# Performance work log

Measured on AMD Instinct MI355X. Metric: run time of the kernel, lower is better.

## Reference

```python
import jax, jax.numpy as jnp
import numpy as np

NEG = -10000.0


def _build_label_vocab():
    vocab = {'O': 0}
    i = 1
    for t in ['PER', 'ORG', 'LOC', 'MISC']:
        for p in ['B', 'I', 'E', 'S']:
            vocab[f'{p}-{t}'] = i
            i += 1
    return vocab


def _init_transition(key):
    """Random transition with BIOES constraints, matching CRF.initialize()."""
    vocab = _build_label_vocab()
    L = len(vocab) + 2          # 19 (17 labels + start + end)
    start, end = L - 2, L - 1
    T = np.array(jax.random.normal(key, (L, L)), dtype=np.float32)
    T[:, end] = NEG
    T[start, :] = NEG
    for lf, i_f in vocab.items():
        pf, tf = ('O', 'O') if lf == 'O' else lf.split('-')
        for lt, i_t in vocab.items():
            pt, tt = ('O', 'O') if lt == 'O' else lt.split('-')
            allowed = (pf in ('O', 'E', 'S') and pt in ('O', 'B', 'S')) or \
                      (pf in ('B', 'I') and pt in ('I', 'E') and tf == tt)
            if not allowed:
                T[i_t, i_f] = NEG
    return jnp.asarray(T)


def setup_inputs() -> dict:
    key = jax.random.key(0)
    k1, k2, k3, k4 = jax.random.split(key, 4)
    B, S, NL = 4096, 256, 17
    logits = jax.random.normal(k1, (B, S, NL), dtype=jnp.float32)
    labels = jax.random.randint(k2, (B, S), 0, NL)
    lens = jax.random.randint(k3, (B,), 1, S + 1)   # lengths in [1, S]
    transition = _init_transition(k4)                # [19, 19]
    return {"logits": logits, "labels": labels, "lens": lens,
            "transition": transition}


def reference(logits, labels, lens, transition):
    """CRF log-likelihood: gold_score(pad_logits(logits)) - norm_score."""
    B, S, NL = logits.shape
    L = transition.shape[0]       # label_size = NL + 2
    start, end = L - 2, L - 1

    # pad_logits: append start/end columns with -10000
    pads = jnp.full((B, S, 2), NEG, dtype=logits.dtype)
    logits_p = jnp.concatenate([logits, pads], axis=2)   # [B, S, L]

    tmask = (jnp.arange(S)[None, :] < lens[:, None])     # [B, S] valid tokens

    # ---- gold score ----
    # unary: gather emission score of the gold label at each position
    unary = jnp.take_along_axis(logits_p, labels[:, :, None], axis=2)[:, :, 0]
    unary = (unary * tmask.astype(logits.dtype)).sum(axis=1)

    # binary: transition scores along the gold path (with start/end padding)
    labels_ext = jnp.concatenate(
        [jnp.full((B, 1), start, labels.dtype), labels,
         jnp.full((B, 1), end, labels.dtype)], axis=1)   # [B, S+2]
    emask = jnp.arange(S + 2)[None, :] < (lens + 1)[:, None]
    labels_ext = jnp.where(emask, labels_ext, end)
    trn_scr = transition[labels_ext[:, 1:], labels_ext[:, :-1]]  # [B, S+1]
    bmask = (jnp.arange(S + 1)[None, :] < (lens + 1)[:, None]).astype(logits.dtype)
    binary = (trn_scr * bmask).sum(axis=1)

    gold = unary + binary

    # ---- partition (norm) score: forward algorithm over time ----
    alpha0 = jnp.full((B, L), NEG, dtype=logits.dtype).at[:, start].set(0.0)

    def step(alpha, xs):
        logit, m = xs  # logit: [B, L], m: [B] bool (position < len)
        # alpha_nxt[b,i] = logit[b,i] + LSE_j(alpha[b,j] + T[i,j])
        nxt = logit + jax.nn.logsumexp(alpha[:, None, :] + transition[None], axis=2)
        alpha = jnp.where(m[:, None], nxt, alpha)
        return alpha, None

    alpha, _ = jax.lax.scan(step, alpha0,
                            (jnp.swapaxes(logits_p, 0, 1), tmask.T))
    alpha = alpha + transition[end][None, :]
    norm = jax.nn.logsumexp(alpha, axis=1)

    return gold - norm   # [B] per-sequence log-likelihood
```

## Files before the change

### kernel.cpp

```cpp
#include <hip/hip_runtime.h>

constexpr int S  = 256;
constexpr int NL = 17;
constexpr int L  = 19;

__global__ __launch_bounds__(64)
void crf_fwd(const float* __restrict__ logits,
             const int*   __restrict__ labels,
             const int*   __restrict__ lens,
             const float* __restrict__ transition,
             float* __restrict__ out)
{
    __shared__ float Tsh[L * L];
    __shared__ __align__(16) float pbuf[2][2][20];

    const int tid  = threadIdx.x;
    const int half = tid >> 5;
    const int lane = tid & 31;
    const int b    = (blockIdx.x << 1) + half;

    for (int k = tid; k < L * L; k += 64) Tsh[k] = transition[k];
    __syncthreads();

    const int  i   = lane;
    const bool act = (i < L);
    const int  ic  = act ? i : 0;

    float Erow[L];
    #pragma unroll
    for (int j = 0; j < L; ++j) Erow[j] = __expf(Tsh[ic * L + j]);

    const int len = lens[b];
    int mlv = max(len, __shfl_xor(len, 32));
    const int maxlen  = __builtin_amdgcn_readfirstlane(mlv);
    const int maxlen8 = (maxlen + 7) & ~7;

    const float* lgp  = logits + (size_t)b * S * NL;
    const int*   labp = labels + (size_t)b * S;

    float p = (i == L - 2) ? 1.0f : 0.0f;
    float m    = 0.0f;
    float utot = 0.0f;
    float btot = 0.0f;
    int prevlab = L - 2;

    float lgbuf[8];
    int   labbuf[8];
    #pragma unroll
    for (int u = 0; u < 8; ++u) {
        lgbuf[u]  = (i < NL) ? lgp[u * NL + i] : 0.0f;
        labbuf[u] = labp[u];
    }

    for (int tb = 0; tb < maxlen8; tb += 8) {
        #pragma unroll
        for (int u = 0; u < 8; ++u) {
            const int   t   = tb + u;
            const float lg  = lgbuf[u];
            const int   lab = labbuf[u];
            const int   tn  = (t + 8 < S) ? (t + 8) : (S - 1);
            lgbuf[u]  = (i < NL) ? lgp[tn * NL + i] : 0.0f;
            labbuf[u] = labp[tn];

            const bool upd = (t < len);

            utot += (upd && i == lab) ? lg : 0.0f;
            const float gtr = Tsh[lab * L + prevlab];
            btot += upd ? gtr : 0.0f;
            prevlab = upd ? lab : prevlab;

            const float el = (i < NL) ? __expf(lg) : 0.0f;

            float* pb = &pbuf[half][u & 1][0];
            if (act) pb[i] = p;
            asm volatile("s_waitcnt lgkmcnt(0)" ::: "memory");
            const float4* q = (const float4*)pb;
            const float4 q0 = q[0], q1 = q[1], q2 = q[2], q3 = q[3], q4 = q[4];

            float a0 = q0.x * Erow[0];
            float a1 = q0.y * Erow[1];
            float a2 = q0.z * Erow[2];
            float a3 = q0.w * Erow[3];
            a0 = fmaf(q1.x, Erow[4],  a0);
            a1 = fmaf(q1.y, Erow[5],  a1);
            a2 = fmaf(q1.z, Erow[6],  a2);
            a3 = fmaf(q1.w, Erow[7],  a3);
            a0 = fmaf(q2.x, Erow[8],  a0);
            a1 = fmaf(q2.y, Erow[9],  a1);
            a2 = fmaf(q2.z, Erow[10], a2);
            a3 = fmaf(q2.w, Erow[11], a3);
            a0 = fmaf(q3.x, Erow[12], a0);
            a1 = fmaf(q3.y, Erow[13], a1);
            a2 = fmaf(q3.z, Erow[14], a2);
            a3 = fmaf(q3.w, Erow[15], a3);
            a0 = fmaf(q4.x, Erow[16], a0);
            a1 = fmaf(q4.y, Erow[17], a1);
            a2 = fmaf(q4.z, Erow[18], a2);

            float v  = (a0 + a1) + (a2 + a3);
            float pn = v * el;

            if ((t & 3) == 3) {
                float m0 = fmaxf(fmaxf(q0.x, q0.y), fmaxf(q0.z, q0.w));
                float m1 = fmaxf(fmaxf(q1.x, q1.y), fmaxf(q1.z, q1.w));
                float m2 = fmaxf(fmaxf(q2.x, q2.y), fmaxf(q2.z, q2.w));
                float m3 = fmaxf(fmaxf(q3.x, q3.y), fmaxf(q3.z, q3.w));
                float m4 = fmaxf(fmaxf(q4.x, q4.y), q4.z);
                float mx = fmaxf(fmaxf(m0, m1), fmaxf(fmaxf(m2, m3), m4));
                pn *= __frcp_rn(mx);
                if (upd) m += __logf(mx);
            }
            p = upd ? pn : p;
        }
    }

    const float Eend = __expf(Tsh[(L - 1) * L + ic]);
    float term = act ? p * Eend : 0.0f;
    #pragma unroll
    for (int off = 16; off >= 1; off >>= 1)
        term += __shfl_xor(term, off, 32);
    const float norm = m + __logf(term);

    #pragma unroll
    for (int off = 16; off >= 1; off >>= 1)
        utot += __shfl_xor(utot, off, 32);
    const int lastlab = labp[len - 1];
    const float gold = utot + btot + Tsh[(L - 1) * L + lastlab];

    if (lane == 0) out[b] = gold - norm;
}

extern "C" void kernel_launch(void* const* d_in, const int* in_sizes, int n_in,
                              void* d_out, int out_size, void* d_ws, size_t ws_size,
                              hipStream_t stream)
{
    (void)n_in; (void)out_size; (void)d_ws; (void)ws_size;
    const float* logits     = (const float*)d_in[0];
    const int*   labels     = (const int*)d_in[1];
    const int*   lens       = (const int*)d_in[2];
    const float* transition = (const float*)d_in[3];
    float*       out        = (float*)d_out;
    const int B = in_sizes[2];
    crf_fwd<<<dim3(B / 2), dim3(64), 0, stream>>>(logits, labels, lens, transition, out);
}
```

Measured before the change: 149.0 us.

## Split each sequence into forward and backward halves computed by two half-waves

Each sequence is now handled by one 64-lane wave instead of one 32-lane half. The first half-wave runs the forward recursion over the first len/2 tokens, and the second half-wave runs a backward recursion from the end token using the transposed transition. The two results are combined with a dot product across halves, and the gold score is also split across the halves. This roughly halves the serial dependency chain per sequence and removes the per-pair max-length imbalance. In exchange it doubles the lane count per sequence, so total thread work and the number of waves launched roughly double.

```diff
diff --git a/kernel.cpp b/kernel.cpp
--- a/kernel.cpp
+++ b/kernel.cpp
@@ -3,8 +3,9 @@
 constexpr int S  = 256;
 constexpr int NL = 17;
 constexpr int L  = 19;
+constexpr int WPB = 2;
 
-__global__ __launch_bounds__(64)
+__global__ __launch_bounds__(64 * WPB)
 void crf_fwd(const float* __restrict__ logits,
              const int*   __restrict__ labels,
              const int*   __restrict__ lens,
@@ -12,93 +13,117 @@
              float* __restrict__ out)
 {
     __shared__ float Tsh[L * L];
-    __shared__ __align__(16) float pbuf[2][2][20];
+    __shared__ __align__(16) float pbuf[WPB][2][2][20];
 
     const int tid  = threadIdx.x;
-    const int half = tid >> 5;
-    const int lane = tid & 31;
-    const int b    = (blockIdx.x << 1) + half;
+    const int wave = tid >> 6;
+    const int wtid = tid & 63;
+    const int half = wtid >> 5;
+    const int lane = wtid & 31;
+    const int b    = blockIdx.x * WPB + wave;
 
-    for (int k = tid; k < L * L; k += 64) Tsh[k] = transition[k];
+    for (int k = tid; k < L * L; k += 64 * WPB) Tsh[k] = transition[k];
     __syncthreads();
 
     const int  i   = lane;
     const bool act = (i < L);
     const int  ic  = act ? i : 0;
 
-    float Erow[L];
+    float coef[L];
     #pragma unroll
-    for (int j = 0; j < L; ++j) Erow[j] = __expf(Tsh[ic * L + j]);
+    for (int j = 0; j < L; ++j)
+        coef[j] = __expf(half ? Tsh[j * L + ic] : Tsh[ic * L + j]);
 
     const int len = lens[b];
-    int mlv = max(len, __shfl_xor(len, 32));
-    const int maxlen  = __builtin_amdgcn_readfirstlane(mlv);
-    const int maxlen8 = (maxlen + 7) & ~7;
+    const int mid = len >> 1;
+    const int nf  = mid;
+    const int nb  = len - mid;
+    const int nup = half ? nb : nf;
+    const int nsteps8 = (nb + 7) & ~7;
 
     const float* lgp  = logits + (size_t)b * S * NL;
     const int*   labp = labels + (size_t)b * S;
 
-    float p = (i == L - 2) ? 1.0f : 0.0f;
+    float p = half ? (act ? __expf(Tsh[(L - 1) * L + ic]) : 0.0f)
+                   : ((i == L - 2) ? 1.0f : 0.0f);
     float m    = 0.0f;
     float utot = 0.0f;
     float btot = 0.0f;
-    int prevlab = L - 2;
+    int   prevF = L - 2;
+
+    if (half) btot = Tsh[(L - 1) * L + labp[len - 1]];
 
     float lgbuf[8];
     int   labbuf[8];
     #pragma unroll
     for (int u = 0; u < 8; ++u) {
-        lgbuf[u]  = (i < NL) ? lgp[u * NL + i] : 0.0f;
-        labbuf[u] = labp[u];
+        int tb0 = len - 1 - u; tb0 = (tb0 > 0) ? tb0 : 0;
+        const int tok = half ? tb0 : u;
+        lgbuf[u]  = (i < NL) ? lgp[tok * NL + i] : 0.0f;
+        labbuf[u] = labp[tok];
     }
 
-    for (int tb = 0; tb < maxlen8; tb += 8) {
+    for (int tb = 0; tb < nsteps8; tb += 8) {
         #pragma unroll
         for (int u = 0; u < 8; ++u) {
             const int   t   = tb + u;
             const float lg  = lgbuf[u];
             const int   lab = labbuf[u];
-            const int   tn  = (t + 8 < S) ? (t + 8) : (S - 1);
-            lgbuf[u]  = (i < NL) ? lgp[tn * NL + i] : 0.0f;
-            labbuf[u] = labp[tn];
+            const int   labnxt = labbuf[(u + 1) & 7];
+            {
+                int tpf = t + 8;       tpf = (tpf < S) ? tpf : (S - 1);
+                int tpb = len - 9 - t; tpb = (tpb > 0) ? tpb : 0;
+                const int tok = half ? tpb : tpf;
+                lgbuf[u]  = (i < NL) ? lgp[tok * NL + i] : 0.0f;
+                labbuf[u] = labp[tok];
+            }
+            const bool upd = (t < nup);
 
-            const bool upd = (t < len);
-
+            int prv;
+            if (half) {
+                const int utok = len - 1 - t;
+                prv = (utok >= 1) ? labnxt : (L - 2);
+            } else {
+                prv = prevF;
+            }
             utot += (upd && i == lab) ? lg : 0.0f;
-            const float gtr = Tsh[lab * L + prevlab];
+            const float gtr = Tsh[lab * L + prv];
             btot += upd ? gtr : 0.0f;
-            prevlab = upd ? lab : prevlab;
+            prevF = upd ? lab : prevF;
 
             const float el = (i < NL) ? __expf(lg) : 0.0f;
+            const float pe = p * el;
+            const float wv = half ? pe : p;
 
-            float* pb = &pbuf[half][u & 1][0];
-            if (act) pb[i] = p;
+            float* pb = &pbuf[wave][half][u & 1][0];
+            if (act) pb[i] = wv;
             asm volatile("s_waitcnt lgkmcnt(0)" ::: "memory");
             const float4* q = (const float4*)pb;
             const float4 q0 = q[0], q1 = q[1], q2 = q[2], q3 = q[3], q4 = q[4];
 
-            float a0 = q0.x * Erow[0];
-            float a1 = q0.y * Erow[1];
-            float a2 = q0.z * Erow[2];
-            float a3 = q0.w * Erow[3];
-            a0 = fmaf(q1.x, Erow[4],  a0);
-            a1 = fmaf(q1.y, Erow[5],  a1);
-            a2 = fmaf(q1.z, Erow[6],  a2);
-            a3 = fmaf(q1.w, Erow[7],  a3);
-            a0 = fmaf(q2.x, Erow[8],  a0);
-            a1 = fmaf(q2.y, Erow[9],  a1);
-            a2 = fmaf(q2.z, Erow[10], a2);
-            a3 = fmaf(q2.w, Erow[11], a3);
-            a0 = fmaf(q3.x, Erow[12], a0);
-            a1 = fmaf(q3.y, Erow[13], a1);
-            a2 = fmaf(q3.z, Erow[14], a2);
-            a3 = fmaf(q3.w, Erow[15], a3);
-            a0 = fmaf(q4.x, Erow[16], a0);
-            a1 = fmaf(q4.y, Erow[17], a1);
-            a2 = fmaf(q4.z, Erow[18], a2);
+            float a0 = q0.x * coef[0];
+            float a1 = q0.y * coef[1];
+            float a2 = q0.z * coef[2];
+            float a3 = q0.w * coef[3];
+            a0 = fmaf(q1.x, coef[4],  a0);
+            a1 = fmaf(q1.y, coef[5],  a1);
+            a2 = fmaf(q1.z, coef[6],  a2);
+            a3 = fmaf(q1.w, coef[7],  a3);
+            a0 = fmaf(q2.x, coef[8],  a0);
+            a1 = fmaf(q2.y, coef[9],  a1);
+            a2 = fmaf(q2.z, coef[10], a2);
+            a3 = fmaf(q2.w, coef[11], a3);
+            a0 = fmaf(q3.x, coef[12], a0);
+            a1 = fmaf(q3.y, coef[13], a1);
+            a2 = fmaf(q3.z, coef[14], a2);
+            a3 = fmaf(q3.w, coef[15], a3);
+            a0 = fmaf(q4.x, coef[16], a0);
+            a1 = fmaf(q4.y, coef[17], a1);
+            a2 = fmaf(q4.z, coef[18], a2);
 
-            float v  = (a0 + a1) + (a2 + a3);
-            float pn = v * el;
+            const float v   = (a0 + a1) + (a2 + a3);
+            const float elf = half ? 1.0f : el;
+            float pn = v * elf;
 
             if ((t & 3) == 3) {
                 float m0 = fmaxf(fmaxf(q0.x, q0.y), fmaxf(q0.z, q0.w));
@@ -114,20 +139,21 @@
         }
     }
 
-    const float Eend = __expf(Tsh[(L - 1) * L + ic]);
-    float term = act ? p * Eend : 0.0f;
+    const float other = __shfl_xor(p, 32);
+    float prod = act ? p * other : 0.0f;
     #pragma unroll
     for (int off = 16; off >= 1; off >>= 1)
-        term += __shfl_xor(term, off, 32);
-    const float norm = m + __logf(term);
+        prod += __shfl_xor(prod, off, 32);
+    const float mtot = m + __shfl_xor(m, 32);
+    const float norm = mtot + __logf(prod);
 
     #pragma unroll
     for (int off = 16; off >= 1; off >>= 1)
         utot += __shfl_xor(utot, off, 32);
-    const int lastlab = labp[len - 1];
-    const float gold = utot + btot + Tsh[(L - 1) * L + lastlab];
+    const float ghalf = utot + btot;
+    const float gold  = ghalf + __shfl_xor(ghalf, 32);
 
-    if (lane == 0) out[b] = gold - norm;
+    if (wtid == 0) out[b] = gold - norm;
 }
 
 extern "C" void kernel_launch(void* const* d_in, const int* in_sizes, int n_in,
@@ -141,5 +167,5 @@
     const float* transition = (const float*)d_in[3];
     float*       out        = (float*)d_out;
     const int B = in_sizes[2];
-    crf_fwd<<<dim3(B / 2), dim3(64), 0, stream>>>(logits, labels, lens, transition, out);
+    crf_fwd<<<dim3(B / WPB), dim3(64 * WPB), 0, stream>>>(logits, labels, lens, transition, out);
 }
```

Result: faster. 140.4 us (-5.8%).
